# Kernel tuning notes

Hardware: AMD Instinct MI355X
Metric: run time of the kernel (lower is better)

The kernel has to match this reference:

```python
import jax, jax.numpy as jnp
import numpy as np

G, M, D = 64, 128, 256  # grid (orig 528), masked len (orig 409), d_model
S = M + 1               # q/k seq len (orig 410)


def setup_inputs() -> dict:
    key = jax.random.key(0)
    ks = jax.random.split(key, 9)
    q = jax.random.normal(ks[0], (1, G, S, D), dtype=jnp.float32)
    k = jax.random.normal(ks[1], (1, G, S, D), dtype=jnp.float32)
    v = jax.random.normal(ks[2], (1, G, M, D), dtype=jnp.float32)
    # binary additive mask (1 = masked out)
    mask = (jax.random.uniform(ks[3], (G, M, M)) > 0.9).astype(jnp.float32)
    scale = 0.05
    Wq = jax.random.normal(ks[4], (D, D), dtype=jnp.float32) * scale
    Wk = jax.random.normal(ks[5], (D, D), dtype=jnp.float32) * scale
    Wv = jax.random.normal(ks[6], (D, D), dtype=jnp.float32) * scale
    Wo = jax.random.normal(ks[7], (D, D), dtype=jnp.float32) * scale
    bq = jnp.zeros((D,), jnp.float32)
    bk = jnp.zeros((D,), jnp.float32)
    bv = jnp.zeros((D,), jnp.float32)
    bo = jnp.zeros((D,), jnp.float32)
    return {"q": q, "k": k, "v": v, "mask": mask,
            "Wq": Wq, "bq": bq, "Wk": Wk, "bk": bk,
            "Wv": Wv, "bv": bv, "Wo": Wo, "bo": bo}


def reference(q, k, v, mask, Wq, bq, Wk, bk, Wv, bv, Wo, bo):
    d = q.shape[-1]
    # dense projections (num_heads=1 so split_heads is a no-op up to squeeze)
    qs = (q @ Wq + bq)[0]   # (G, S, D)
    ks_ = (k @ Wk + bk)[0]  # (G, S, D)
    vs = (v @ Wv + bv)[0]   # (G, M, D)
    # 2D QK^T over all grid-row pairs: tensordot->squeeze->transpose in orig
    scores = jnp.einsum('aid,bjd->abij', qs, ks_)  # (G, G, S, S)
    scores = scores[:, :, 1:, :-1]                 # (G, G, M, M)
    nl_qk = scores / jnp.sqrt(jnp.asarray(d, jnp.float32))
    nl_qk = nl_qk + mask[:, None, :, :] * (-1e9)   # repeat mask over axis 1
    # idiosyncratic flattened softmax: reshape to (M, G*G*M), softmax, reshape back
    att = jax.nn.softmax(nl_qk.reshape(M, -1), axis=-1).reshape(G, G, M, M)
    # contract att axes [1,3] with v axes [0,1]
    out = jnp.einsum('abmc,bcd->amd', att, vs)     # (G, M, D)
    output = out @ Wo + bo                          # (G, M, D)
    return output, att
```

## Files before the change

### kernel.cpp

```cpp
#include <hip/hip_runtime.h>
#include <hip/hip_bf16.h>

#define G 64
#define M 128
#define D 256
#define S 129

typedef short s16x8 __attribute__((ext_vector_type(8)));
typedef float f32x4 __attribute__((ext_vector_type(4)));

__device__ inline void gld16(const void* g, void* l) {
    __builtin_amdgcn_global_load_lds(
        (const __attribute__((address_space(1))) unsigned int*)g,
        (__attribute__((address_space(3))) unsigned int*)l, 16, 0, 0);
}

__device__ inline unsigned short f2bf(float f) {
    __hip_bfloat16 h = __float2bfloat16(f);
    return *reinterpret_cast<unsigned short*>(&h);
}

#define BM 64
#define BN 64
#define BK 16
#define PAD 4
__global__ __launch_bounds__(256) void proj_bf16(const float* __restrict__ src,
                                                 const float* __restrict__ W,
                                                 const float* __restrict__ bias,
                                                 unsigned short* __restrict__ dstb,
                                                 int outer, int off) {
    __shared__ float As[BK][BM + PAD];
    __shared__ float Bs[BK][BN + PAD];
    const int tid = threadIdx.x;
    const int tx = tid & 15, ty = tid >> 4;
    const int m0 = blockIdx.y * BM;
    const int n0 = blockIdx.x * BN;
    const int lr = tid >> 2;
    const int lc = (tid & 3) * 4;
    const int arow = m0 + lr;
    const int asrc_row = (arow >> 7) * outer + (arow & 127) + off;
    const float* aptr = src + (size_t)asrc_row * D;
    const int br = tid >> 4;
    const int bc = (tid & 15) * 4;

    float acc[4][4] = {};
    for (int k0 = 0; k0 < D; k0 += BK) {
        float4 av = *(const float4*)(aptr + k0 + lc);
        As[lc + 0][lr] = av.x; As[lc + 1][lr] = av.y;
        As[lc + 2][lr] = av.z; As[lc + 3][lr] = av.w;
        float4 bv = *(const float4*)(W + (size_t)(k0 + br) * D + n0 + bc);
        *(float4*)&Bs[br][bc] = bv;
        __syncthreads();
#pragma unroll
        for (int kk = 0; kk < BK; ++kk) {
            float4 a4 = *(const float4*)&As[kk][ty * 4];
            float4 b4 = *(const float4*)&Bs[kk][tx * 4];
            float ar[4] = {a4.x, a4.y, a4.z, a4.w};
            float brr[4] = {b4.x, b4.y, b4.z, b4.w};
#pragma unroll
            for (int i = 0; i < 4; ++i)
#pragma unroll
                for (int j = 0; j < 4; ++j)
                    acc[i][j] = fmaf(ar[i], brr[j], acc[i][j]);
        }
        __syncthreads();
    }
    float4 bb = *(const float4*)(bias + n0 + tx * 4);
#pragma unroll
    for (int i = 0; i < 4; ++i) {
        int row = m0 + ty * 4 + i;
        ushort4 o;
        o.x = f2bf(acc[i][0] + bb.x);
        o.y = f2bf(acc[i][1] + bb.y);
        o.z = f2bf(acc[i][2] + bb.z);
        o.w = f2bf(acc[i][3] + bb.w);
        *(ushort4*)(dstb + (size_t)row * D + n0 + tx * 4) = o;
    }
}

__global__ __launch_bounds__(256) void projo_kernel(const float* __restrict__ s0,
                                                    const float* __restrict__ s1,
                                                    const float* __restrict__ W,
                                                    const float* __restrict__ bias,
                                                    float* __restrict__ dst) {
    __shared__ float As[BK][BM + PAD];
    __shared__ float Bs[BK][BN + PAD];
    const int tid = threadIdx.x;
    const int tx = tid & 15, ty = tid >> 4;
    const int m0 = blockIdx.y * BM;
    const int n0 = blockIdx.x * BN;
    const int lr = tid >> 2;
    const int lc = (tid & 3) * 4;
    const int br = tid >> 4;
    const int bc = (tid & 15) * 4;

    float acc[4][4] = {};
    for (int k0 = 0; k0 < D; k0 += BK) {
        float4 a0 = *(const float4*)(s0 + (size_t)(m0 + lr) * D + k0 + lc);
        float4 a1 = *(const float4*)(s1 + (size_t)(m0 + lr) * D + k0 + lc);
        As[lc + 0][lr] = a0.x + a1.x; As[lc + 1][lr] = a0.y + a1.y;
        As[lc + 2][lr] = a0.z + a1.z; As[lc + 3][lr] = a0.w + a1.w;
        float4 bv = *(const float4*)(W + (size_t)(k0 + br) * D + n0 + bc);
        *(float4*)&Bs[br][bc] = bv;
        __syncthreads();
#pragma unroll
        for (int kk = 0; kk < BK; ++kk) {
            float4 a4 = *(const float4*)&As[kk][ty * 4];
            float4 b4 = *(const float4*)&Bs[kk][tx * 4];
            float ar[4] = {a4.x, a4.y, a4.z, a4.w};
            float brr[4] = {b4.x, b4.y, b4.z, b4.w};
#pragma unroll
            for (int i = 0; i < 4; ++i)
#pragma unroll
                for (int j = 0; j < 4; ++j)
                    acc[i][j] = fmaf(ar[i], brr[j], acc[i][j]);
        }
        __syncthreads();
    }
    float4 bb = *(const float4*)(bias + n0 + tx * 4);
#pragma unroll
    for (int i = 0; i < 4; ++i) {
        int row = m0 + ty * 4 + i;
        float4 o;
        o.x = acc[i][0] + bb.x; o.y = acc[i][1] + bb.y;
        o.z = acc[i][2] + bb.z; o.w = acc[i][3] + bb.w;
        *(float4*)(dst + (size_t)row * D + n0 + tx * 4) = o;
    }
}

__global__ __launch_bounds__(256) void transpose_kernel(const unsigned short* __restrict__ in,
                                                        unsigned short* __restrict__ out) {
    __shared__ unsigned short t[64][68];
    const int c0 = blockIdx.x * 64;
    const int r0 = blockIdx.y * 64;
    const int lr = threadIdx.x >> 4;
    const int lc = (threadIdx.x & 15) * 4;
#pragma unroll
    for (int p = 0; p < 4; ++p) {
        int row = p * 16 + lr;
        ushort4 v = *(const ushort4*)(in + (size_t)(r0 + row) * D + c0 + lc);
        t[lc + 0][row] = v.x; t[lc + 1][row] = v.y;
        t[lc + 2][row] = v.z; t[lc + 3][row] = v.w;
    }
    __syncthreads();
#pragma unroll
    for (int p = 0; p < 4; ++p) {
        int dr = p * 16 + lr;
        ushort4 v = *(const ushort4*)(&t[dr][lc]);
        *(ushort4*)(out + (size_t)(c0 + dr) * (G * M) + r0 + lc) = v;
    }
}

__global__ __launch_bounds__(256) void scores_mfma(const unsigned short* __restrict__ Qb,
                                                   const unsigned short* __restrict__ Kb,
                                                   const float* __restrict__ mask,
                                                   float* __restrict__ att,
                                                   float* __restrict__ row_sum) {
    __shared__ __align__(16) char sm[32768];
    const int tid = threadIdx.x;
    const int ab = blockIdx.x;
    const int a = ab >> 6, b = ab & 63;
    const int w = tid >> 6, l = tid & 63;
    const int wi = w >> 1, wj = w & 1;

    const unsigned short* qbase = Qb + (size_t)a * M * D;
    const unsigned short* kbase = Kb + (size_t)b * M * D;

    const int s0 = tid, s1 = tid + 256;
    const int r0s = s0 >> 2, r1s = s1 >> 2;
    const int g0 = (((s0 & 3) ^ ((r0s >> 1) & 3)) * 8);
    const int g1 = (((s1 & 3) ^ ((r1s >> 1) & 3)) * 8);
    const int slotp = (((l >> 4) ^ (((l & 15) >> 1) & 3)) << 4);

    f32x4 acc[4][4] = {};

#define SC_STAGE(buf, t)                                                        \
    do {                                                                        \
        int k0 = (t) * 32;                                                      \
        gld16(qbase + (size_t)r0s * D + k0 + g0, sm + (buf)*8192 + s0 * 16);    \
        gld16(qbase + (size_t)r1s * D + k0 + g1, sm + (buf)*8192 + s1 * 16);    \
        gld16(kbase + (size_t)r0s * D + k0 + g0, sm + 16384 + (buf)*8192 + s0 * 16); \
        gld16(kbase + (size_t)r1s * D + k0 + g1, sm + 16384 + (buf)*8192 + s1 * 16); \
    } while (0)

    SC_STAGE(0, 0);
    __syncthreads();
    for (int t = 0; t < 8; ++t) {
        const int buf = t & 1;
        if (t < 7) SC_STAGE(buf ^ 1, t + 1);
        s16x8 af[4], bf[4];
#pragma unroll
        for (int f = 0; f < 4; ++f) {
            af[f] = *(const s16x8*)(sm + buf * 8192 + (wi * 64 + f * 16 + (l & 15)) * 64 + slotp);
            bf[f] = *(const s16x8*)(sm + 16384 + buf * 8192 + (wj * 64 + f * 16 + (l & 15)) * 64 + slotp);
        }
#pragma unroll
        for (int i = 0; i < 4; ++i)
#pragma unroll
            for (int j = 0; j < 4; ++j)
                acc[i][j] = __builtin_amdgcn_mfma_f32_16x16x32_bf16(af[i], bf[j], acc[i][j], 0, 0, 0);
        __syncthreads();
    }

    float tsum = 0.f;
    const int ro = (l >> 4) * 4;
    const int co = l & 15;
#pragma unroll
    for (int i = 0; i < 4; ++i)
#pragma unroll
        for (int j = 0; j < 4; ++j) {
            const int jj = wj * 64 + j * 16 + co;
#pragma unroll
            for (int r = 0; r < 4; ++r) {
                const int ii = wi * 64 + i * 16 + ro + r;
                float val = acc[i][j][r] * 0.0625f;
                float mv = mask[((size_t)a * M + ii) * M + jj];
                float e = __expf(fmaf(mv, -1e9f, val));
                tsum += e;
                att[(((size_t)(a * G + b)) * M + ii) * M + jj] = e;
            }
        }
    __syncthreads();
    float* red = (float*)sm;
    red[tid] = tsum;
    __syncthreads();
    for (int st = 128; st > 0; st >>= 1) {
        if (tid < st) red[tid] += red[tid + st];
        __syncthreads();
    }
    if (tid == 0) atomicAdd(&row_sum[2 * a + (b >> 5)], red[0]);
}

__global__ void inv_kernel(const float* __restrict__ rs, float* __restrict__ inv) {
    int t = threadIdx.x;
    if (t < 2 * G) inv[t] = 1.0f / rs[t];
}

__global__ __launch_bounds__(256) void pv_mfma(float* __restrict__ att,
                                               const unsigned short* __restrict__ Vt,
                                               const float* __restrict__ invb,
                                               float* __restrict__ P0,
                                               float* __restrict__ P1) {
    __shared__ __align__(16) char sm[36864];
    const int tid = threadIdx.x;
    const int bh = blockIdx.x;
    const int i0 = blockIdx.y * 32;
    const int a = blockIdx.z;
    const int w = tid >> 6, l = tid & 63;
    const float iv = invb[2 * a + bh];
    float* __restrict__ Pb = bh ? P1 : P0;

    const int ar = tid >> 3, aq = tid & 7;
    const int awbyte = ar * 64 + (((aq >> 1) ^ ((ar >> 1) & 3)) << 4) + (aq & 1) * 8;
    const int slotp = (((l >> 4) ^ (((l & 15) >> 1) & 3)) << 4);

    f32x4 acc[2][4] = {};

    size_t aoff_t = 0;
#define PV_AADDR(t) (att + ((size_t)(a * G + bh * 32 + ((t) >> 2)) * M + i0 + ar) * M + ((t) & 3) * 32 + aq * 4)

    auto BSTAGE = [&](int t) {
        const int buf = t & 1;
        const int kbase = bh * 4096 + t * 32;
#pragma unroll
        for (int k2 = 0; k2 < 4; ++k2) {
            int s = tid + 256 * k2;
            int d = s >> 2;
            int gsl = (((s & 3) ^ ((d >> 1) & 3)) * 8);
            gld16(Vt + (size_t)d * (G * M) + kbase + gsl, sm + 4096 + buf * 16384 + s * 16);
        }
    };
    auto AFIN = [&](int t, f32x4 v) {
        f32x4 wv = v * iv;
        *(f32x4*)PV_AADDR(t) = wv;
        unsigned long long pk = (unsigned long long)f2bf(wv[0]) |
                                ((unsigned long long)f2bf(wv[1]) << 16) |
                                ((unsigned long long)f2bf(wv[2]) << 32) |
                                ((unsigned long long)f2bf(wv[3]) << 48);
        *(unsigned long long*)(sm + (t & 1) * 2048 + awbyte) = pk;
    };

    {
        f32x4 av = *(const f32x4*)PV_AADDR(0);
        BSTAGE(0);
        AFIN(0, av);
    }
    __syncthreads();

    for (int t = 0; t < 128; ++t) {
        const int buf = t & 1;
        f32x4 nv;
        if (t < 127) {
            nv = *(const f32x4*)PV_AADDR(t + 1);
            BSTAGE(t + 1);
        }
        s16x8 af[2], bf[4];
#pragma unroll
        for (int f = 0; f < 2; ++f)
            af[f] = *(const s16x8*)(sm + buf * 2048 + (f * 16 + (l & 15)) * 64 + slotp);
#pragma unroll
        for (int f = 0; f < 4; ++f)
            bf[f] = *(const s16x8*)(sm + 4096 + buf * 16384 + (w * 64 + f * 16 + (l & 15)) * 64 + slotp);
#pragma unroll
        for (int i = 0; i < 2; ++i)
#pragma unroll
            for (int j = 0; j < 4; ++j)
                acc[i][j] = __builtin_amdgcn_mfma_f32_16x16x32_bf16(af[i], bf[j], acc[i][j], 0, 0, 0);
        if (t < 127) AFIN(t + 1, nv);
        __syncthreads();
    }

#pragma unroll
    for (int i = 0; i < 2; ++i)
#pragma unroll
        for (int j = 0; j < 4; ++j)
#pragma unroll
            for (int r = 0; r < 4; ++r) {
                const int ii = i0 + i * 16 + (l >> 4) * 4 + r;
                const int dd = w * 64 + j * 16 + (l & 15);
                Pb[((size_t)a * M + ii) * D + dd] = acc[i][j][r];
            }
}

extern "C" void kernel_launch(void* const* d_in, const int* in_sizes, int n_in,
                              void* d_out, int out_size, void* d_ws, size_t ws_size,
                              hipStream_t stream) {
    const float* q    = (const float*)d_in[0];
    const float* k    = (const float*)d_in[1];
    const float* v    = (const float*)d_in[2];
    const float* mask = (const float*)d_in[3];
    const float* Wq   = (const float*)d_in[4];
    const float* bq   = (const float*)d_in[5];
    const float* Wk   = (const float*)d_in[6];
    const float* bk   = (const float*)d_in[7];
    const float* Wv   = (const float*)d_in[8];
    const float* bv   = (const float*)d_in[9];
    const float* Wo   = (const float*)d_in[10];
    const float* bo   = (const float*)d_in[11];

    float* out = (float*)d_out;
    float* att = out + (size_t)G * M * D;

    const size_t NE = (size_t)G * M * D;
    unsigned short* Qbf = (unsigned short*)d_ws;
    unsigned short* Kbf = Qbf + NE;
    unsigned short* Vbf = Kbf + NE;
    unsigned short* Vt  = Vbf + NE;
    float* row_sum = (float*)Vbf;
    float* invb    = row_sum + 128;
    float* P0 = (float*)d_ws;
    float* P1 = (float*)((char*)d_ws + (size_t)16 * 1024 * 1024);

    dim3 blk(256);
    dim3 gproj(D / BN, (G * M) / BM);
    proj_bf16<<<gproj, blk, 0, stream>>>(q, Wq, bq, Qbf, S, 1);
    proj_bf16<<<gproj, blk, 0, stream>>>(k, Wk, bk, Kbf, S, 0);
    proj_bf16<<<gproj, blk, 0, stream>>>(v, Wv, bv, Vbf, M, 0);

    transpose_kernel<<<dim3(D / 64, (G * M) / 64), blk, 0, stream>>>(Vbf, Vt);

    hipMemsetAsync(row_sum, 0, 2 * G * sizeof(float), stream);

    scores_mfma<<<dim3(G * G), blk, 0, stream>>>(Qbf, Kbf, mask, att, row_sum);

    inv_kernel<<<1, 128, 0, stream>>>(row_sum, invb);

    pv_mfma<<<dim3(2, 4, G), blk, 0, stream>>>(att, Vt, invb, P0, P1);

    projo_kernel<<<gproj, blk, 0, stream>>>(P0, P1, Wo, bo, out);
}
```

Baseline: 749.0 us.

## Move projections to bf16 MFMA and retile the PV kernel

The inputs are converted to bf16 and the weights are transposed to bf16 up front. The fp32 SIMT projection GEMMs are then replaced with MFMA kernels, and the V projection writes its output already transposed, so the separate transpose kernel is removed. The PV kernel is rebuilt with 512-thread blocks, 64-row tiles and larger k-steps with XOR-swizzled LDS, which should improve reuse and cut loop iterations. The output projection also uses MFMA, with P0+P1 summed and converted to bf16 on the fly. In exchange it adds seven small conversion launches and lowers the precision of the projection inputs to bf16.

```diff
diff --git a/kernel.cpp b/kernel.cpp
--- a/kernel.cpp
+++ b/kernel.cpp
@@ -20,117 +20,18 @@
     return *reinterpret_cast<unsigned short*>(&h);
 }
 
-#define BM 64
-#define BN 64
-#define BK 16
-#define PAD 4
-__global__ __launch_bounds__(256) void proj_bf16(const float* __restrict__ src,
-                                                 const float* __restrict__ W,
-                                                 const float* __restrict__ bias,
-                                                 unsigned short* __restrict__ dstb,
-                                                 int outer, int off) {
-    __shared__ float As[BK][BM + PAD];
-    __shared__ float Bs[BK][BN + PAD];
-    const int tid = threadIdx.x;
-    const int tx = tid & 15, ty = tid >> 4;
-    const int m0 = blockIdx.y * BM;
-    const int n0 = blockIdx.x * BN;
-    const int lr = tid >> 2;
-    const int lc = (tid & 3) * 4;
-    const int arow = m0 + lr;
-    const int asrc_row = (arow >> 7) * outer + (arow & 127) + off;
-    const float* aptr = src + (size_t)asrc_row * D;
-    const int br = tid >> 4;
-    const int bc = (tid & 15) * 4;
-
-    float acc[4][4] = {};
-    for (int k0 = 0; k0 < D; k0 += BK) {
-        float4 av = *(const float4*)(aptr + k0 + lc);
-        As[lc + 0][lr] = av.x; As[lc + 1][lr] = av.y;
-        As[lc + 2][lr] = av.z; As[lc + 3][lr] = av.w;
-        float4 bv = *(const float4*)(W + (size_t)(k0 + br) * D + n0 + bc);
-        *(float4*)&Bs[br][bc] = bv;
-        __syncthreads();
-#pragma unroll
-        for (int kk = 0; kk < BK; ++kk) {
-            float4 a4 = *(const float4*)&As[kk][ty * 4];
-            float4 b4 = *(const float4*)&Bs[kk][tx * 4];
-            float ar[4] = {a4.x, a4.y, a4.z, a4.w};
-            float brr[4] = {b4.x, b4.y, b4.z, b4.w};
-#pragma unroll
-            for (int i = 0; i < 4; ++i)
-#pragma unroll
-                for (int j = 0; j < 4; ++j)
-                    acc[i][j] = fmaf(ar[i], brr[j], acc[i][j]);
-        }
-        __syncthreads();
-    }
-    float4 bb = *(const float4*)(bias + n0 + tx * 4);
-#pragma unroll
-    for (int i = 0; i < 4; ++i) {
-        int row = m0 + ty * 4 + i;
-        ushort4 o;
-        o.x = f2bf(acc[i][0] + bb.x);
-        o.y = f2bf(acc[i][1] + bb.y);
-        o.z = f2bf(acc[i][2] + bb.z);
-        o.w = f2bf(acc[i][3] + bb.w);
-        *(ushort4*)(dstb + (size_t)row * D + n0 + tx * 4) = o;
-    }
-}
-
-__global__ __launch_bounds__(256) void projo_kernel(const float* __restrict__ s0,
-                                                    const float* __restrict__ s1,
-                                                    const float* __restrict__ W,
-                                                    const float* __restrict__ bias,
-                                                    float* __restrict__ dst) {
-    __shared__ float As[BK][BM + PAD];
-    __shared__ float Bs[BK][BN + PAD];
-    const int tid = threadIdx.x;
-    const int tx = tid & 15, ty = tid >> 4;
-    const int m0 = blockIdx.y * BM;
-    const int n0 = blockIdx.x * BN;
-    const int lr = tid >> 2;
-    const int lc = (tid & 3) * 4;
-    const int br = tid >> 4;
-    const int bc = (tid & 15) * 4;
-
-    float acc[4][4] = {};
-    for (int k0 = 0; k0 < D; k0 += BK) {
-        float4 a0 = *(const float4*)(s0 + (size_t)(m0 + lr) * D + k0 + lc);
-        float4 a1 = *(const float4*)(s1 + (size_t)(m0 + lr) * D + k0 + lc);
-        As[lc + 0][lr] = a0.x + a1.x; As[lc + 1][lr] = a0.y + a1.y;
-        As[lc + 2][lr] = a0.z + a1.z; As[lc + 3][lr] = a0.w + a1.w;
-        float4 bv = *(const float4*)(W + (size_t)(k0 + br) * D + n0 + bc);
-        *(float4*)&Bs[br][bc] = bv;
-        __syncthreads();
-#pragma unroll
-        for (int kk = 0; kk < BK; ++kk) {
-            float4 a4 = *(const float4*)&As[kk][ty * 4];
-            float4 b4 = *(const float4*)&Bs[kk][tx * 4];
-            float ar[4] = {a4.x, a4.y, a4.z, a4.w};
-            float brr[4] = {b4.x, b4.y, b4.z, b4.w};
-#pragma unroll
-            for (int i = 0; i < 4; ++i)
-#pragma unroll
-                for (int j = 0; j < 4; ++j)
-                    acc[i][j] = fmaf(ar[i], brr[j], acc[i][j]);
-        }
-        __syncthreads();
-    }
-    float4 bb = *(const float4*)(bias + n0 + tx * 4);
-#pragma unroll
-    for (int i = 0; i < 4; ++i) {
-        int row = m0 + ty * 4 + i;
-        float4 o;
-        o.x = acc[i][0] + bb.x; o.y = acc[i][1] + bb.y;
-        o.z = acc[i][2] + bb.z; o.w = acc[i][3] + bb.w;
-        *(float4*)(dst + (size_t)row * D + n0 + tx * 4) = o;
-    }
-}
-
-__global__ __launch_bounds__(256) void transpose_kernel(const unsigned short* __restrict__ in,
-                                                        unsigned short* __restrict__ out) {
-    __shared__ unsigned short t[64][68];
+__global__ __launch_bounds__(256) void cvt_kernel(const float* __restrict__ src,
+                                                  unsigned short* __restrict__ dst, int n4) {
+    int i = blockIdx.x * 256 + threadIdx.x;
+    if (i >= n4) return;
+    float4 v = ((const float4*)src)[i];
+    ushort4 o = {f2bf(v.x), f2bf(v.y), f2bf(v.z), f2bf(v.w)};
+    ((ushort4*)dst)[i] = o;
+}
+
+__global__ __launch_bounds__(256) void wt_kernel(const float* __restrict__ in,
+                                                 unsigned short* __restrict__ out) {
+    __shared__ float t[64][68];
     const int c0 = blockIdx.x * 64;
     const int r0 = blockIdx.y * 64;
     const int lr = threadIdx.x >> 4;
@@ -138,7 +39,7 @@
 #pragma unroll
     for (int p = 0; p < 4; ++p) {
         int row = p * 16 + lr;
-        ushort4 v = *(const ushort4*)(in + (size_t)(r0 + row) * D + c0 + lc);
+        float4 v = *(const float4*)(in + (size_t)(r0 + row) * D + c0 + lc);
         t[lc + 0][row] = v.x; t[lc + 1][row] = v.y;
         t[lc + 2][row] = v.z; t[lc + 3][row] = v.w;
     }
@@ -146,9 +47,82 @@
 #pragma unroll
     for (int p = 0; p < 4; ++p) {
         int dr = p * 16 + lr;
-        ushort4 v = *(const ushort4*)(&t[dr][lc]);
-        *(ushort4*)(out + (size_t)(c0 + dr) * (G * M) + r0 + lc) = v;
-    }
+        ushort4 o = {f2bf(t[dr][lc]), f2bf(t[dr][lc + 1]), f2bf(t[dr][lc + 2]), f2bf(t[dr][lc + 3])};
+        *(ushort4*)(out + (size_t)(c0 + dr) * D + r0 + lc) = o;
+    }
+}
+
+__global__ __launch_bounds__(256) void proj_mfma(const unsigned short* __restrict__ src,
+                                                 const unsigned short* __restrict__ WT,
+                                                 const float* __restrict__ bias,
+                                                 unsigned short* __restrict__ dst,
+                                                 int outer, int off, int transposed) {
+    __shared__ __align__(16) char sm[24576];
+    const int tid = threadIdx.x;
+    const int w = tid >> 6, l = tid & 63;
+    const int wi = w >> 1, wj = w & 1;
+    const int m0 = blockIdx.y * 128;
+    const int n0 = blockIdx.x * 64;
+
+    const int s0 = tid, s1 = tid + 256;
+    const int ar0 = s0 >> 2, ar1 = s1 >> 2;
+    const int g0 = (((s0 & 3) ^ ((ar0 >> 1) & 3)) * 8);
+    const int g1 = (((s1 & 3) ^ ((ar1 >> 1) & 3)) * 8);
+    const int am0 = m0 + ar0, am1 = m0 + ar1;
+    const size_t asrc0 = (size_t)((am0 >> 7) * outer + (am0 & 127) + off) * D;
+    const size_t asrc1 = (size_t)((am1 >> 7) * outer + (am1 & 127) + off) * D;
+    const int brw = tid >> 2;
+    const int gb = (((tid & 3) ^ ((brw >> 1) & 3)) * 8);
+    const size_t bsrc = (size_t)(n0 + brw) * D;
+    const int slotp = (((l >> 4) ^ (((l & 15) >> 1) & 3)) << 4);
+
+    f32x4 acc[4][2] = {};
+
+#define PJ_STAGE(buf, t)                                                  \
+    do {                                                                  \
+        int k0 = (t) * 32;                                                \
+        gld16(src + asrc0 + k0 + g0, sm + (buf)*8192 + s0 * 16);          \
+        gld16(src + asrc1 + k0 + g1, sm + (buf)*8192 + s1 * 16);          \
+        gld16(WT + bsrc + k0 + gb, sm + 16384 + (buf)*4096 + tid * 16);   \
+    } while (0)
+
+    PJ_STAGE(0, 0);
+    __syncthreads();
+    for (int t = 0; t < 8; ++t) {
+        const int buf = t & 1;
+        if (t < 7) PJ_STAGE(buf ^ 1, t + 1);
+        s16x8 af[4], bfr[2];
+#pragma unroll
+        for (int f = 0; f < 4; ++f)
+            af[f] = *(const s16x8*)(sm + buf * 8192 + (wi * 64 + f * 16 + (l & 15)) * 64 + slotp);
+#pragma unroll
+        for (int f = 0; f < 2; ++f)
+            bfr[f] = *(const s16x8*)(sm + 16384 + buf * 4096 + (wj * 32 + f * 16 + (l & 15)) * 64 + slotp);
+#pragma unroll
+        for (int i = 0; i < 4; ++i)
+#pragma unroll
+            for (int j = 0; j < 2; ++j)
+                acc[i][j] = __builtin_amdgcn_mfma_f32_16x16x32_bf16(af[i], bfr[j], acc[i][j], 0, 0, 0);
+        __syncthreads();
+    }
+
+#pragma unroll
+    for (int i = 0; i < 4; ++i)
+#pragma unroll
+        for (int j = 0; j < 2; ++j) {
+            const int col = n0 + wj * 32 + j * 16 + (l & 15);
+            const int row0 = m0 + wi * 64 + i * 16 + (l >> 4) * 4;
+            const float bb = bias[col];
+            if (transposed) {
+                ushort4 o = {f2bf(acc[i][j][0] + bb), f2bf(acc[i][j][1] + bb),
+                             f2bf(acc[i][j][2] + bb), f2bf(acc[i][j][3] + bb)};
+                *(ushort4*)(dst + (size_t)col * (G * M) + row0) = o;
+            } else {
+#pragma unroll
+                for (int r = 0; r < 4; ++r)
+                    dst[(size_t)(row0 + r) * D + col] = f2bf(acc[i][j][r] + bb);
+            }
+        }
 }
 
 __global__ __launch_bounds__(256) void scores_mfma(const unsigned short* __restrict__ Qb,
@@ -188,17 +162,17 @@
     for (int t = 0; t < 8; ++t) {
         const int buf = t & 1;
         if (t < 7) SC_STAGE(buf ^ 1, t + 1);
-        s16x8 af[4], bf[4];
+        s16x8 af[4], bfr[4];
 #pragma unroll
         for (int f = 0; f < 4; ++f) {
             af[f] = *(const s16x8*)(sm + buf * 8192 + (wi * 64 + f * 16 + (l & 15)) * 64 + slotp);
-            bf[f] = *(const s16x8*)(sm + 16384 + buf * 8192 + (wj * 64 + f * 16 + (l & 15)) * 64 + slotp);
+            bfr[f] = *(const s16x8*)(sm + 16384 + buf * 8192 + (wj * 64 + f * 16 + (l & 15)) * 64 + slotp);
         }
 #pragma unroll
         for (int i = 0; i < 4; ++i)
 #pragma unroll
             for (int j = 0; j < 4; ++j)
-                acc[i][j] = __builtin_amdgcn_mfma_f32_16x16x32_bf16(af[i], bf[j], acc[i][j], 0, 0, 0);
+                acc[i][j] = __builtin_amdgcn_mfma_f32_16x16x32_bf16(af[i], bfr[j], acc[i][j], 0, 0, 0);
         __syncthreads();
     }
 
@@ -236,77 +210,73 @@
     if (t < 2 * G) inv[t] = 1.0f / rs[t];
 }
 
-__global__ __launch_bounds__(256) void pv_mfma(float* __restrict__ att,
-                                               const unsigned short* __restrict__ Vt,
-                                               const float* __restrict__ invb,
-                                               float* __restrict__ P0,
-                                               float* __restrict__ P1) {
-    __shared__ __align__(16) char sm[36864];
+__global__ __launch_bounds__(512) void pv2(float* __restrict__ att,
+                                           const unsigned short* __restrict__ Vt,
+                                           const float* __restrict__ invb,
+                                           float* __restrict__ P0,
+                                           float* __restrict__ P1) {
+    __shared__ __align__(16) char sm[81920];
     const int tid = threadIdx.x;
-    const int bh = blockIdx.x;
-    const int i0 = blockIdx.y * 32;
-    const int a = blockIdx.z;
+    const int kh = blockIdx.x, ih = blockIdx.y, a = blockIdx.z;
     const int w = tid >> 6, l = tid & 63;
-    const float iv = invb[2 * a + bh];
-    float* __restrict__ Pb = bh ? P1 : P0;
-
-    const int ar = tid >> 3, aq = tid & 7;
-    const int awbyte = ar * 64 + (((aq >> 1) ^ ((ar >> 1) & 3)) << 4) + (aq & 1) * 8;
-    const int slotp = (((l >> 4) ^ (((l & 15) >> 1) & 3)) << 4);
-
+    const int wr = w >> 2, wc = w & 3;
+    const float iv = invb[2 * a + kh];
+    float* __restrict__ Pb = kh ? P1 : P0;
+
+    const int arow = tid >> 3, aslot = tid & 7;
+    const int ajsw = ((aslot ^ (arow & 7)) * 8);
     f32x4 acc[2][4] = {};
 
-    size_t aoff_t = 0;
-#define PV_AADDR(t) (att + ((size_t)(a * G + bh * 32 + ((t) >> 2)) * M + i0 + ar) * M + ((t) & 3) * 32 + aq * 4)
-
-    auto BSTAGE = [&](int t) {
-        const int buf = t & 1;
-        const int kbase = bh * 4096 + t * 32;
-#pragma unroll
-        for (int k2 = 0; k2 < 4; ++k2) {
-            int s = tid + 256 * k2;
-            int d = s >> 2;
-            int gsl = (((s & 3) ^ ((d >> 1) & 3)) * 8);
-            gld16(Vt + (size_t)d * (G * M) + kbase + gsl, sm + 4096 + buf * 16384 + s * 16);
+#define PV_STAGE(buf, hp)                                                           \
+    do {                                                                            \
+        const int p_ = (hp) >> 1, kb_ = ((hp) & 1) * 64;                            \
+        _Pragma("unroll")                                                           \
+        for (int u = 0; u < 4; ++u) {                                               \
+            int cb = u * 512 + tid;                                                 \
+            int brow = cb >> 3, bslot = cb & 7;                                     \
+            gld16(Vt + (size_t)brow * (G * M) + kh * 4096 + p_ * 128 + kb_ +        \
+                      ((bslot ^ (brow & 7)) * 8),                                   \
+                  sm + 16384 + (buf)*32768 + cb * 16);                              \
+        }                                                                           \
+        float* ap = att + (((size_t)(a * G + kh * 32 + p_) * M) + ih * 64 + arow) * M + kb_ + ajsw; \
+        float4 v0 = *(float4*)ap;                                                   \
+        float4 v1 = *(float4*)(ap + 4);                                             \
+        float4 w0 = {v0.x * iv, v0.y * iv, v0.z * iv, v0.w * iv};                   \
+        float4 w1 = {v1.x * iv, v1.y * iv, v1.z * iv, v1.w * iv};                   \
+        *(float4*)ap = w0;                                                          \
+        *(float4*)(ap + 4) = w1;                                                    \
+        union { ushort4 h[2]; uint4 q; } pk;                                        \
+        pk.h[0] = (ushort4){f2bf(w0.x), f2bf(w0.y), f2bf(w0.z), f2bf(w0.w)};        \
+        pk.h[1] = (ushort4){f2bf(w1.x), f2bf(w1.y), f2bf(w1.z), f2bf(w1.w)};        \
+        *(uint4*)(sm + (buf)*8192 + tid * 16) = pk.q;                               \
+    } while (0)
+
+    PV_STAGE(0, 0);
+    __syncthreads();
+    for (int hp = 0; hp < 64; ++hp) {
+        const int buf = hp & 1;
+        if (hp < 63) PV_STAGE(buf ^ 1, hp + 1);
+#pragma unroll
+        for (int ks = 0; ks < 2; ++ks) {
+            s16x8 af[2], bfr[4];
+#pragma unroll
+            for (int f = 0; f < 2; ++f) {
+                int row = wr * 32 + f * 16 + (l & 15);
+                int sl = (ks * 4 + (l >> 4)) ^ (row & 7);
+                af[f] = *(const s16x8*)(sm + buf * 8192 + row * 128 + sl * 16);
+            }
+#pragma unroll
+            for (int f = 0; f < 4; ++f) {
+                int row = wc * 64 + f * 16 + (l & 15);
+                int sl = (ks * 4 + (l >> 4)) ^ (row & 7);
+                bfr[f] = *(const s16x8*)(sm + 16384 + buf * 32768 + row * 128 + sl * 16);
+            }
+#pragma unroll
+            for (int i = 0; i < 2; ++i)
+#pragma unroll
+                for (int j = 0; j < 4; ++j)
+                    acc[i][j] = __builtin_amdgcn_mfma_f32_16x16x32_bf16(af[i], bfr[j], acc[i][j], 0, 0, 0);
         }
-    };
-    auto AFIN = [&](int t, f32x4 v) {
-        f32x4 wv = v * iv;
-        *(f32x4*)PV_AADDR(t) = wv;
-        unsigned long long pk = (unsigned long long)f2bf(wv[0]) |
-                                ((unsigned long long)f2bf(wv[1]) << 16) |
-                                ((unsigned long long)f2bf(wv[2]) << 32) |
-                                ((unsigned long long)f2bf(wv[3]) << 48);
-        *(unsigned long long*)(sm + (t & 1) * 2048 + awbyte) = pk;
-    };
-
-    {
-        f32x4 av = *(const f32x4*)PV_AADDR(0);
-        BSTAGE(0);
-        AFIN(0, av);
-    }
-    __syncthreads();
-
-    for (int t = 0; t < 128; ++t) {
-        const int buf = t & 1;
-        f32x4 nv;
-        if (t < 127) {
-            nv = *(const f32x4*)PV_AADDR(t + 1);
-            BSTAGE(t + 1);
-        }
-        s16x8 af[2], bf[4];
-#pragma unroll
-        for (int f = 0; f < 2; ++f)
-            af[f] = *(const s16x8*)(sm + buf * 2048 + (f * 16 + (l & 15)) * 64 + slotp);
-#pragma unroll
-        for (int f = 0; f < 4; ++f)
-            bf[f] = *(const s16x8*)(sm + 4096 + buf * 16384 + (w * 64 + f * 16 + (l & 15)) * 64 + slotp);
-#pragma unroll
-        for (int i = 0; i < 2; ++i)
-#pragma unroll
-            for (int j = 0; j < 4; ++j)
-                acc[i][j] = __builtin_amdgcn_mfma_f32_16x16x32_bf16(af[i], bf[j], acc[i][j], 0, 0, 0);
-        if (t < 127) AFIN(t + 1, nv);
         __syncthreads();
     }
 
@@ -316,10 +286,85 @@
         for (int j = 0; j < 4; ++j)
 #pragma unroll
             for (int r = 0; r < 4; ++r) {
-                const int ii = i0 + i * 16 + (l >> 4) * 4 + r;
-                const int dd = w * 64 + j * 16 + (l & 15);
+                const int ii = ih * 64 + wr * 32 + i * 16 + (l >> 4) * 4 + r;
+                const int dd = wc * 64 + j * 16 + (l & 15);
                 Pb[((size_t)a * M + ii) * D + dd] = acc[i][j][r];
             }
+}
+
+__global__ __launch_bounds__(256) void projo_mfma(const float* __restrict__ P0,
+                                                  const float* __restrict__ P1,
+                                                  const unsigned short* __restrict__ WT,
+                                                  const float* __restrict__ bias,
+                                                  float* __restrict__ dst) {
+    __shared__ __align__(16) char sm[24576];
+    const int tid = threadIdx.x;
+    const int w = tid >> 6, l = tid & 63;
+    const int wi = w >> 1, wj = w & 1;
+    const int m0 = blockIdx.y * 128;
+    const int n0 = blockIdx.x * 64;
+
+    const int s0 = tid, s1 = tid + 256;
+    const int ar0 = s0 >> 2, ar1 = s1 >> 2;
+    const int g0 = (((s0 & 3) ^ ((ar0 >> 1) & 3)) * 8);
+    const int g1 = (((s1 & 3) ^ ((ar1 >> 1) & 3)) * 8);
+    const int brw = tid >> 2;
+    const int gb = (((tid & 3) ^ ((brw >> 1) & 3)) * 8);
+    const size_t bsrc = (size_t)(n0 + brw) * D;
+    const int slotp = (((l >> 4) ^ (((l & 15) >> 1) & 3)) << 4);
+
+    f32x4 acc[4][2] = {};
+
+#define PO_STAGE(buf, t)                                                        \
+    do {                                                                        \
+        int k0 = (t) * 32;                                                      \
+        gld16(WT + bsrc + k0 + gb, sm + 16384 + (buf)*4096 + tid * 16);         \
+        size_t f0 = (size_t)(m0 + ar0) * D + k0 + g0;                           \
+        size_t f1 = (size_t)(m0 + ar1) * D + k0 + g1;                           \
+        float4 a0 = *(const float4*)(P0 + f0), a1 = *(const float4*)(P0 + f0 + 4); \
+        float4 b0 = *(const float4*)(P1 + f0), b1 = *(const float4*)(P1 + f0 + 4); \
+        float4 c0 = *(const float4*)(P0 + f1), c1 = *(const float4*)(P0 + f1 + 4); \
+        float4 d0 = *(const float4*)(P1 + f1), d1 = *(const float4*)(P1 + f1 + 4); \
+        union { ushort4 h[2]; uint4 q; } pa, pb;                                \
+        pa.h[0] = (ushort4){f2bf(a0.x + b0.x), f2bf(a0.y + b0.y), f2bf(a0.z + b0.z), f2bf(a0.w + b0.w)}; \
+        pa.h[1] = (ushort4){f2bf(a1.x + b1.x), f2bf(a1.y + b1.y), f2bf(a1.z + b1.z), f2bf(a1.w + b1.w)}; \
+        pb.h[0] = (ushort4){f2bf(c0.x + d0.x), f2bf(c0.y + d0.y), f2bf(c0.z + d0.z), f2bf(c0.w + d0.w)}; \
+        pb.h[1] = (ushort4){f2bf(c1.x + d1.x), f2bf(c1.y + d1.y), f2bf(c1.z + d1.z), f2bf(c1.w + d1.w)}; \
+        *(uint4*)(sm + (buf)*8192 + s0 * 16) = pa.q;                            \
+        *(uint4*)(sm + (buf)*8192 + s1 * 16) = pb.q;                            \
+    } while (0)
+
+    PO_STAGE(0, 0);
+    __syncthreads();
+    for (int t = 0; t < 8; ++t) {
+        const int buf = t & 1;
+        if (t < 7) PO_STAGE(buf ^ 1, t + 1);
+        s16x8 af[4], bfr[2];
+#pragma unroll
+        for (int f = 0; f < 4; ++f)
+            af[f] = *(const s16x8*)(sm + buf * 8192 + (wi * 64 + f * 16 + (l & 15)) * 64 + slotp);
+#pragma unroll
+        for (int f = 0; f < 2; ++f)
+            bfr[f] = *(const s16x8*)(sm + 16384 + buf * 4096 + (wj * 32 + f * 16 + (l & 15)) * 64 + slotp);
+#pragma unroll
+        for (int i = 0; i < 4; ++i)
+#pragma unroll
+            for (int j = 0; j < 2; ++j)
+                acc[i][j] = __builtin_amdgcn_mfma_f32_16x16x32_bf16(af[i], bfr[j], acc[i][j], 0, 0, 0);
+        __syncthreads();
+    }
+
+#pragma unroll
+    for (int i = 0; i < 4; ++i)
+#pragma unroll
+        for (int j = 0; j < 2; ++j) {
+            const int col = n0 + wj * 32 + j * 16 + (l & 15);
+            const int row0 = m0 + wi * 64 + i * 16 + (l >> 4) * 4;
+            const float bb = bias[col];
+#pragma unroll
+            for (int r = 0; r < 4; ++r)
+                dst[(size_t)(row0 + r) * D + col] = acc[i][j][r] + bb;
+        }
 }
 
 extern "C" void kernel_launch(void* const* d_in, const int* in_sizes, int n_in,
@@ -341,31 +386,45 @@
     float* out = (float*)d_out;
     float* att = out + (size_t)G * M * D;
 
-    const size_t NE = (size_t)G * M * D;
-    unsigned short* Qbf = (unsigned short*)d_ws;
-    unsigned short* Kbf = Qbf + NE;
-    unsigned short* Vbf = Kbf + NE;
-    unsigned short* Vt  = Vbf + NE;
-    float* row_sum = (float*)Vbf;
-    float* invb    = row_sum + 128;
-    float* P0 = (float*)d_ws;
-    float* P1 = (float*)((char*)d_ws + (size_t)16 * 1024 * 1024);
+    char* ws = (char*)d_ws;
+    unsigned short* qb  = (unsigned short*)(ws + 0);
+    unsigned short* kb  = (unsigned short*)(ws + 4227072);
+    unsigned short* vb  = (unsigned short*)(ws + 8454144);
+    unsigned short* WqT = (unsigned short*)(ws + 12648448);
+    unsigned short* WkT = (unsigned short*)(ws + 12648448 + 131072);
+    unsigned short* WvT = (unsigned short*)(ws + 12648448 + 262144);
+    unsigned short* WoT = (unsigned short*)(ws + 12648448 + 393216);
+    unsigned short* Qbf = (unsigned short*)(ws + 13172736);
+    unsigned short* Kbf = (unsigned short*)(ws + 17367040);
+    unsigned short* Vt  = (unsigned short*)(ws + 21561344);
+    float* P0      = (float*)(ws + 0);
+    float* P1      = (float*)(ws + 25755648);
+    float* row_sum = (float*)(ws + 34144256);
+    float* invb    = (float*)(ws + 34144768);
 
     dim3 blk(256);
-    dim3 gproj(D / BN, (G * M) / BM);
-    proj_bf16<<<gproj, blk, 0, stream>>>(q, Wq, bq, Qbf, S, 1);
-    proj_bf16<<<gproj, blk, 0, stream>>>(k, Wk, bk, Kbf, S, 0);
-    proj_bf16<<<gproj, blk, 0, stream>>>(v, Wv, bv, Vbf, M, 0);
-
-    transpose_kernel<<<dim3(D / 64, (G * M) / 64), blk, 0, stream>>>(Vbf, Vt);
+    const int nq4 = (G * S * D) / 4;
+    const int nv4 = (G * M * D) / 4;
+    cvt_kernel<<<(nq4 + 255) / 256, blk, 0, stream>>>(q, qb, nq4);
+    cvt_kernel<<<(nq4 + 255) / 256, blk, 0, stream>>>(k, kb, nq4);
+    cvt_kernel<<<(nv4 + 255) / 256, blk, 0, stream>>>(v, vb, nv4);
+    wt_kernel<<<dim3(4, 4), blk, 0, stream>>>(Wq, WqT);
+    wt_kernel<<<dim3(4, 4), blk, 0, stream>>>(Wk, WkT);
+    wt_kernel<<<dim3(4, 4), blk, 0, stream>>>(Wv, WvT);
+    wt_kernel<<<dim3(4, 4), blk, 0, stream>>>(Wo, WoT);
 
     hipMemsetAsync(row_sum, 0, 2 * G * sizeof(float), stream);
 
+    dim3 gproj(D / 64, (G * M) / 128);
+    proj_mfma<<<gproj, blk, 0, stream>>>(qb, WqT, bq, Qbf, S, 1, 0);
+    proj_mfma<<<gproj, blk, 0, stream>>>(kb, WkT, bk, Kbf, S, 0, 0);
+    proj_mfma<<<gproj, blk, 0, stream>>>(vb, WvT, bv, Vt, M, 0, 1);
+
     scores_mfma<<<dim3(G * G), blk, 0, stream>>>(Qbf, Kbf, mask, att, row_sum);
 
     inv_kernel<<<1, 128, 0, stream>>>(row_sum, invb);
 
-    pv_mfma<<<dim3(2, 4, G), blk, 0, stream>>>(att, Vt, invb, P0, P1);
-
-    projo_kernel<<<gproj, blk, 0, stream>>>(P0, P1, Wo, bo, out);
-}
+    pv2<<<dim3(2, 2, G), dim3(512), 0, stream>>>(att, Vt, invb, P0, P1);
+
+    projo_mfma<<<gproj, blk, 0, stream>>>(P0, P1, WoT, bo, out);
+}
```

Result: faster. 667.7 us (-10.9%).
